# Kernel tuning notes

Measured on AMD Instinct MI355X. Metric: run time of the kernel, lower is better.

The kernel has to match this reference:

```python
import jax, jax.numpy as jnp
import numpy as np

TOPK = 2
NORM_TOPK = True
SCALE = 1.0
EPS = 1e-9


def setup_inputs() -> dict:
    key = jax.random.key(0)
    ks = jax.random.split(key, 9)
    h, i, E = 2048, 1024, 16
    std = 0.02
    return {
        "x": jax.random.normal(ks[0], (1, 2048, h), jnp.float32),
        "Wr": jax.random.normal(ks[1], (E, h), jnp.float32) * std,
        "bias": jnp.zeros((E,), jnp.float32),
        "Wg": jax.random.normal(ks[2], (E, h, i), jnp.float32) * std,
        "Wu": jax.random.normal(ks[3], (E, h, i), jnp.float32) * std,
        "Wd": jax.random.normal(ks[4], (E, i, h), jnp.float32) * std,
        "sWg": jax.random.normal(ks[5], (h, i), jnp.float32) * std,
        "sWu": jax.random.normal(ks[6], (h, i), jnp.float32) * std,
        "sWd": jax.random.normal(ks[7], (i, h), jnp.float32) * std,
    }


def reference(x, Wr, bias, Wg, Wu, Wd, sWg, sWu, sWd):
    b, s, h = x.shape
    E = Wr.shape[0]
    xt = x.reshape(b * s, h)  # [T, h]

    # Router: softmax over expert logits, then top-k
    logits = xt @ Wr.T + bias  # [T, E]
    probs = jax.nn.softmax(logits, axis=-1)
    topk_val, topk_idx = jax.lax.top_k(probs, TOPK)  # [T, K]
    if NORM_TOPK:
        w = topk_val / (jnp.sum(topk_val, axis=-1, keepdims=True) + EPS)
    else:
        w = topk_val
    w = w * SCALE

    # Dense per-expert SwiGLU (mathematically identical to gather/scatter dispatch)
    g = jnp.einsum('th,ehi->tei', xt, Wg)  # [T, E, i]
    u = jnp.einsum('th,ehi->tei', xt, Wu)
    y = jnp.einsum('tei,eih->teh', jax.nn.silu(g) * u, Wd)  # [T, E, h]

    # Combine: out[t] = sum_k w[t,k] * y[t, idx[t,k]]
    oh = jax.nn.one_hot(topk_idx, E, dtype=x.dtype)  # [T, K, E]
    routed = jnp.einsum('tke,tk,teh->th', oh, w, y)

    # Shared expert (SwiGLU)
    shared = (jax.nn.silu(xt @ sWg) * (xt @ sWu)) @ sWd

    return (routed + shared).reshape(b, s, h)
```

## Files before the change

### kernel.cpp

```cpp
#include <hip/hip_runtime.h>
#include <hip/hip_bf16.h>

#define T_TOK 2048
#define HDIM  2048
#define IDIM  1024
#define NE    16
#define NEX   17
#define NASSIGN (T_TOK*3)

#define G1_RT 16
#define G1_NCT 8
#define G2_RT 16
#define G2_NCT 16

typedef __attribute__((ext_vector_type(8))) short bf16x8;
typedef __attribute__((ext_vector_type(4))) float f32x4;

__device__ __forceinline__ unsigned short f2bf(float f) {
    union { float f; unsigned u; } v; v.f = f;
    unsigned r = v.u + 0x7fffu + ((v.u >> 16) & 1u);
    return (unsigned short)(r >> 16);
}
__device__ __forceinline__ unsigned pack2f(float a, float b) {
    __hip_bfloat162 h = __float22bfloat162_rn(float2{a, b});
    unsigned r;
    __builtin_memcpy(&r, &h, 4);
    return r;
}
__device__ __forceinline__ float fidx(const float4& v, int j) {
    return ((const float*)&v)[j];
}
__device__ __forceinline__ int SW(int r) { return (r ^ (r >> 2)) & 7; }
__device__ __forceinline__ int lds_off(int row, int kelem) {
    return (row << 7) + ((((kelem >> 3) ^ SW(row))) << 4) + ((kelem & 7) << 1);
}
__device__ __forceinline__ f32x4 mfma16(bf16x8 a, bf16x8 b, f32x4 c) {
    return __builtin_amdgcn_mfma_f32_16x16x32_bf16(a, b, c, 0, 0, 0);
}
__device__ __forceinline__ void gload_lds16(const void* g, void* lds) {
    __builtin_amdgcn_global_load_lds(
        (const __attribute__((address_space(1))) unsigned*)g,
        (__attribute__((address_space(3))) unsigned*)lds, 16, 0, 0);
}

__global__ __launch_bounds__(256) void k_cvt(const float* __restrict__ x,
                                             unsigned short* __restrict__ xbf) {
    int i = blockIdx.x * 256 + threadIdx.x;
    float4 v = ((const float4*)x)[i];
    uint2 p{pack2f(v.x, v.y), pack2f(v.z, v.w)};
    ((uint2*)xbf)[i] = p;
}

__global__ void k_router(const float* __restrict__ x, const float* __restrict__ Wr,
                         const float* __restrict__ bias, float* __restrict__ wtok,
                         int* __restrict__ idxtok, int* __restrict__ counts) {
    int t = blockIdx.x;
    int lane = threadIdx.x & 63;
    int wave = threadIdx.x >> 6;
    __shared__ float lg[NE];
    const float4* xr = (const float4*)(x + (size_t)t * HDIM);
    for (int e = wave; e < NE; e += 4) {
        const float4* wr = (const float4*)(Wr + (size_t)e * HDIM);
        float s = 0.f;
        for (int j = lane; j < HDIM / 4; j += 64) {
            float4 a = xr[j], b = wr[j];
            s += a.x*b.x + a.y*b.y + a.z*b.z + a.w*b.w;
        }
        #pragma unroll
        for (int d = 32; d; d >>= 1) s += __shfl_xor(s, d);
        if (lane == 0) lg[e] = s + bias[e];
    }
    __syncthreads();
    if (threadIdx.x == 0) {
        float m = lg[0];
        #pragma unroll
        for (int e = 1; e < NE; e++) m = fmaxf(m, lg[e]);
        float p[NE]; float S = 0.f;
        #pragma unroll
        for (int e = 0; e < NE; e++) { p[e] = expf(lg[e] - m); S += p[e]; }
        int i0 = 0;
        #pragma unroll
        for (int e = 1; e < NE; e++) if (p[e] > p[i0]) i0 = e;
        int i1 = (i0 == 0) ? 1 : 0;
        for (int e = 0; e < NE; e++) if (e != i0 && p[e] > p[i1]) i1 = e;
        float v0 = p[i0] / S, v1 = p[i1] / S;
        float wsum = v0 + v1 + 1e-9f;
        wtok[t*2+0] = v0 / wsum;
        wtok[t*2+1] = v1 / wsum;
        idxtok[t*2+0] = i0;
        idxtok[t*2+1] = i1;
        atomicAdd(&counts[i0], 1);
        atomicAdd(&counts[i1], 1);
    }
}

__global__ void k_scan(const int* __restrict__ counts, int* __restrict__ offs,
                       int* __restrict__ cursor) {
    if (threadIdx.x == 0) {
        int acc = 0;
        for (int e = 0; e < NEX; e++) {
            offs[e] = acc; cursor[e] = acc;
            acc += (e < NE) ? counts[e] : T_TOK;
        }
        offs[NEX] = acc;
    }
}

__global__ void k_scatter(const int* __restrict__ idxtok, const float* __restrict__ wtok,
                          int* __restrict__ cursor, const int* __restrict__ offs,
                          int* __restrict__ rows, float* __restrict__ wrow) {
    int t = blockIdx.x * blockDim.x + threadIdx.x;
    if (t >= T_TOK) return;
    #pragma unroll
    for (int k = 0; k < 2; k++) {
        int e = idxtok[t*2+k];
        int pos = atomicAdd(&cursor[e], 1);
        rows[pos] = t;
        wrow[pos] = wtok[t*2+k];
    }
    int p16 = offs[NE] + t;
    rows[p16] = t;
    wrow[p16] = 1.0f;
}

__global__ __launch_bounds__(512) void k_gemm1(
        const unsigned short* __restrict__ xbf,
        const float* __restrict__ Wg, const float* __restrict__ Wu,
        const float* __restrict__ sWg, const float* __restrict__ sWu,
        const int* __restrict__ offs, const int* __restrict__ rows,
        const float* __restrict__ wrow, unsigned short* __restrict__ act) {
    const int nwg = G1_NCT * NEX * G1_RT;
    int bid = blockIdx.x;
    int wg = (bid & 7) * (nwg >> 3) + (bid >> 3);
    int rt = wg & (G1_RT - 1);
    int rest = wg >> 4;
    int e = rest % NEX;
    int ct = rest / NEX;

    int rs = offs[e] + rt * 128;
    int re = offs[e + 1];
    if (rs >= re) return;
    int nrows = min(128, re - rs);
    const float* wgp = (e < NE) ? Wg + (size_t)e * HDIM * IDIM : sWg;
    const float* wup = (e < NE) ? Wu + (size_t)e * HDIM * IDIM : sWu;
    int n0 = ct * 128;

    __shared__ unsigned short As[128 * 64];
    __shared__ unsigned short Bs[128 * 64];
    __shared__ unsigned short Us[128 * 64];
    __shared__ int rloc[128];

    int tid = threadIdx.x;
    if (tid < 128) rloc[tid] = rows[rs + min(tid, nrows - 1)];
    __syncthreads();

    int l = tid & 63, w = tid >> 6;
    int ar0 = w * 8 + (l >> 3);
    int ar1 = 64 + ar0;
    int ac = l & 7;
    const unsigned short* asrc0 = xbf + (size_t)rloc[ar0] * HDIM + ((ac ^ SW(ar0)) << 3);
    const unsigned short* asrc1 = xbf + (size_t)rloc[ar1] * HDIM + ((ac ^ SW(ar1)) << 3);

    int n4 = (tid & 31) << 2;
    int k4 = (tid >> 5) << 2;
    const float* gsrc = wgp + (size_t)k4 * IDIM + n0 + n4;
    const float* usrc = wup + (size_t)k4 * IDIM + n0 + n4;

    int wr = (w >> 2) << 6;
    int wc = (w & 3) << 5;
    int fr = l & 15;
    int fk = (l >> 4) << 3;

    f32x4 accg[4][2] = {}, accu[4][2] = {};

    for (int k0 = 0; k0 < HDIM; k0 += 64) {
        float4 gv[4], uv[4];
        #pragma unroll
        for (int j = 0; j < 4; ++j) gv[j] = *(const float4*)(gsrc + (size_t)(k0 + j) * IDIM);
        #pragma unroll
        for (int j = 0; j < 4; ++j) uv[j] = *(const float4*)(usrc + (size_t)(k0 + j) * IDIM);

        __syncthreads();
        gload_lds16(asrc0 + k0, (char*)As + w * 1024);
        gload_lds16(asrc1 + k0, (char*)As + 8192 + w * 1024);
        #pragma unroll
        for (int i = 0; i < 4; ++i) {
            int n = n4 + i;
            int off = (n << 7) + ((((k4 >> 3) ^ SW(n))) << 4) + ((k4 & 4) << 1);
            uint2 pg{pack2f(fidx(gv[0], i), fidx(gv[1], i)), pack2f(fidx(gv[2], i), fidx(gv[3], i))};
            uint2 pu{pack2f(fidx(uv[0], i), fidx(uv[1], i)), pack2f(fidx(uv[2], i), fidx(uv[3], i))};
            *(uint2*)((char*)Bs + off) = pg;
            *(uint2*)((char*)Us + off) = pu;
        }
        __syncthreads();

        #pragma unroll
        for (int kh = 0; kh < 2; ++kh) {
            int kk = (kh << 5) + fk;
            bf16x8 a[4], bg[2], bu[2];
            #pragma unroll
            for (int m = 0; m < 4; ++m)
                a[m] = *(const bf16x8*)((const char*)As + lds_off(wr + m * 16 + fr, kk));
            #pragma unroll
            for (int n = 0; n < 2; ++n) {
                bg[n] = *(const bf16x8*)((const char*)Bs + lds_off(wc + n * 16 + fr, kk));
                bu[n] = *(const bf16x8*)((const char*)Us + lds_off(wc + n * 16 + fr, kk));
            }
            #pragma unroll
            for (int m = 0; m < 4; ++m) {
                #pragma unroll
                for (int n = 0; n < 2; ++n) {
                    accg[m][n] = mfma16(a[m], bg[n], accg[m][n]);
                    accu[m][n] = mfma16(a[m], bu[n], accu[m][n]);
                }
            }
        }
    }

    int crow = (l >> 4) << 2;
    int ccol = l & 15;
    #pragma unroll
    for (int m = 0; m < 4; ++m) {
        #pragma unroll
        for (int reg = 0; reg < 4; ++reg) {
            int r = wr + m * 16 + crow + reg;
            if (r < nrows) {
                float wv = wrow[rs + r];
                size_t base = (size_t)(rs + r) * IDIM + n0 + wc + ccol;
                #pragma unroll
                for (int n = 0; n < 2; ++n) {
                    float g = accg[m][n][reg], u = accu[m][n][reg];
                    act[base + n * 16] = f2bf(g / (1.f + __expf(-g)) * u * wv);
                }
            }
        }
    }
}

__global__ __launch_bounds__(512) void k_gemm2(
        const unsigned short* __restrict__ act,
        const float* __restrict__ Wd, const float* __restrict__ sWd,
        const int* __restrict__ offs, const int* __restrict__ rows,
        float* __restrict__ out) {
    const int nwg = G2_NCT * NEX * G2_RT;
    int bid = blockIdx.x;
    int wg = (bid & 7) * (nwg >> 3) + (bid >> 3);
    int rt = wg & (G2_RT - 1);
    int rest = wg >> 4;
    int e = rest % NEX;
    int ct = rest / NEX;

    int rs = offs[e] + rt * 128;
    int re = offs[e + 1];
    if (rs >= re) return;
    int nrows = min(128, re - rs);
    const float* wdp = (e < NE) ? Wd + (size_t)e * IDIM * HDIM : sWd;
    int n0 = ct * 128;

    __shared__ unsigned short As[128 * 64];
    __shared__ unsigned short Bs[128 * 64];
    __shared__ int rloc[128];

    int tid = threadIdx.x;
    if (tid < 128) rloc[tid] = rows[rs + min(tid, nrows - 1)];

    int l = tid & 63, w = tid >> 6;
    int ar0 = w * 8 + (l >> 3);
    int ar1 = 64 + ar0;
    int ac = l & 7;
    const unsigned short* asrc0 = act + (size_t)(rs + ar0) * IDIM + ((ac ^ SW(ar0)) << 3);
    const unsigned short* asrc1 = act + (size_t)(rs + ar1) * IDIM + ((ac ^ SW(ar1)) << 3);

    int n4 = (tid & 31) << 2;
    int k4 = (tid >> 5) << 2;
    const float* dsrc = wdp + (size_t)k4 * HDIM + n0 + n4;

    int wr = (w >> 2) << 6;
    int wc = (w & 3) << 5;
    int fr = l & 15;
    int fk = (l >> 4) << 3;

    f32x4 acc[4][2] = {};
    __syncthreads();

    for (int k0 = 0; k0 < IDIM; k0 += 64) {
        float4 dv[4];
        #pragma unroll
        for (int j = 0; j < 4; ++j) dv[j] = *(const float4*)(dsrc + (size_t)(k0 + j) * HDIM);

        __syncthreads();
        gload_lds16(asrc0 + k0, (char*)As + w * 1024);
        gload_lds16(asrc1 + k0, (char*)As + 8192 + w * 1024);
        #pragma unroll
        for (int i = 0; i < 4; ++i) {
            int n = n4 + i;
            int off = (n << 7) + ((((k4 >> 3) ^ SW(n))) << 4) + ((k4 & 4) << 1);
            uint2 pd{pack2f(fidx(dv[0], i), fidx(dv[1], i)), pack2f(fidx(dv[2], i), fidx(dv[3], i))};
            *(uint2*)((char*)Bs + off) = pd;
        }
        __syncthreads();

        #pragma unroll
        for (int kh = 0; kh < 2; ++kh) {
            int kk = (kh << 5) + fk;
            bf16x8 a[4], b[2];
            #pragma unroll
            for (int m = 0; m < 4; ++m)
                a[m] = *(const bf16x8*)((const char*)As + lds_off(wr + m * 16 + fr, kk));
            #pragma unroll
            for (int n = 0; n < 2; ++n)
                b[n] = *(const bf16x8*)((const char*)Bs + lds_off(wc + n * 16 + fr, kk));
            #pragma unroll
            for (int m = 0; m < 4; ++m) {
                #pragma unroll
                for (int n = 0; n < 2; ++n)
                    acc[m][n] = mfma16(a[m], b[n], acc[m][n]);
            }
        }
    }

    int crow = (l >> 4) << 2;
    int ccol = l & 15;
    #pragma unroll
    for (int m = 0; m < 4; ++m) {
        #pragma unroll
        for (int reg = 0; reg < 4; ++reg) {
            int r = wr + m * 16 + crow + reg;
            if (r < nrows) {
                size_t base = (size_t)rloc[r] * HDIM + n0 + wc + ccol;
                atomicAdd(&out[base], acc[m][0][reg]);
                atomicAdd(&out[base + 16], acc[m][1][reg]);
            }
        }
    }
}

extern "C" void kernel_launch(void* const* d_in, const int* in_sizes, int n_in,
                              void* d_out, int out_size, void* d_ws, size_t ws_size,
                              hipStream_t stream) {
    const float* x    = (const float*)d_in[0];
    const float* Wr   = (const float*)d_in[1];
    const float* bias = (const float*)d_in[2];
    const float* Wg   = (const float*)d_in[3];
    const float* Wu   = (const float*)d_in[4];
    const float* Wd   = (const float*)d_in[5];
    const float* sWg  = (const float*)d_in[6];
    const float* sWu  = (const float*)d_in[7];
    const float* sWd  = (const float*)d_in[8];
    float* out = (float*)d_out;

    char* p = (char*)d_ws;
    int*   counts = (int*)p;                 p += 256;
    int*   offs   = (int*)p;                 p += 256;
    int*   cursor = (int*)p;                 p += 256;
    int*   idxtok = (int*)p;                 p += (size_t)T_TOK * 2 * sizeof(int);
    float* wtok   = (float*)p;               p += (size_t)T_TOK * 2 * sizeof(float);
    int*   rows   = (int*)p;                 p += (size_t)NASSIGN * sizeof(int);
    float* wrow   = (float*)p;               p += (size_t)NASSIGN * sizeof(float);
    unsigned short* act = (unsigned short*)p; p += (size_t)NASSIGN * IDIM * sizeof(unsigned short);
    unsigned short* xbf = (unsigned short*)p;

    hipMemsetAsync(counts, 0, 256, stream);
    hipMemsetAsync(d_out, 0, (size_t)out_size * sizeof(float), stream);

    k_cvt<<<dim3(T_TOK * HDIM / 1024), dim3(256), 0, stream>>>(x, xbf);
    k_router<<<dim3(T_TOK), dim3(256), 0, stream>>>(x, Wr, bias, wtok, idxtok, counts);
    k_scan<<<dim3(1), dim3(64), 0, stream>>>(counts, offs, cursor);
    k_scatter<<<dim3((T_TOK + 255) / 256), dim3(256), 0, stream>>>(idxtok, wtok, cursor, offs, rows, wrow);
    k_gemm1<<<dim3(G1_NCT * NEX * G1_RT), dim3(512), 0, stream>>>(xbf, Wg, Wu, sWg, sWu, offs, rows, wrow, act);
    k_gemm2<<<dim3(G2_NCT * NEX * G2_RT), dim3(512), 0, stream>>>(act, Wd, sWd, offs, rows, out);
}
```

Before: 367.8 us.

## Compact tile list, double-buffer LDS, and narrow column tiles in MoE GEMMs

The scan kernel now builds a compact list of 128-row tiles across experts, so GEMM grids launch only real tiles instead of a padded expert-by-row-tile grid full of early-exit blocks. Both GEMMs switch from async global-to-LDS loads to register-staged double buffering: the next K slice is prefetched into registers while MFMAs run on the current LDS buffer. Column tiles shrink from 128 to 64, which doubles the number of workgroups for better CU occupancy. The cost is that each weight tile is reused over fewer columns and the A tile is loaded more often.

```diff
diff --git a/kernel.cpp b/kernel.cpp
--- a/kernel.cpp
+++ b/kernel.cpp
@@ -7,11 +7,12 @@
 #define NE    16
 #define NEX   17
 #define NASSIGN (T_TOK*3)
-
-#define G1_RT 16
-#define G1_NCT 8
-#define G2_RT 16
-#define G2_NCT 16
+#define TM    64
+
+#define G1_NCT 16
+#define G2_NCT 32
+#define G1_NWG (TM*G1_NCT)
+#define G2_NWG (TM*G2_NCT)
 
 typedef __attribute__((ext_vector_type(8))) short bf16x8;
 typedef __attribute__((ext_vector_type(4))) float f32x4;
@@ -36,11 +37,6 @@
 }
 __device__ __forceinline__ f32x4 mfma16(bf16x8 a, bf16x8 b, f32x4 c) {
     return __builtin_amdgcn_mfma_f32_16x16x32_bf16(a, b, c, 0, 0, 0);
-}
-__device__ __forceinline__ void gload_lds16(const void* g, void* lds) {
-    __builtin_amdgcn_global_load_lds(
-        (const __attribute__((address_space(1))) unsigned*)g,
-        (__attribute__((address_space(3))) unsigned*)lds, 16, 0, 0);
 }
 
 __global__ __launch_bounds__(256) void k_cvt(const float* __restrict__ x,
@@ -95,7 +91,7 @@
 }
 
 __global__ void k_scan(const int* __restrict__ counts, int* __restrict__ offs,
-                       int* __restrict__ cursor) {
+                       int* __restrict__ cursor, int4* __restrict__ tiles) {
     if (threadIdx.x == 0) {
         int acc = 0;
         for (int e = 0; e < NEX; e++) {
@@ -103,6 +99,14 @@
             acc += (e < NE) ? counts[e] : T_TOK;
         }
         offs[NEX] = acc;
+        int nt = 0;
+        for (int e = 0; e < NEX; e++) {
+            for (int r = offs[e]; r < offs[e+1]; r += 128) {
+                tiles[nt] = int4{r, min(128, offs[e+1] - r), e, 0};
+                nt++;
+            }
+        }
+        for (; nt < TM; nt++) tiles[nt] = int4{0, 0, 0, 0};
     }
 }
 
@@ -127,93 +131,96 @@
         const unsigned short* __restrict__ xbf,
         const float* __restrict__ Wg, const float* __restrict__ Wu,
         const float* __restrict__ sWg, const float* __restrict__ sWu,
-        const int* __restrict__ offs, const int* __restrict__ rows,
+        const int4* __restrict__ tiles, const int* __restrict__ rows,
         const float* __restrict__ wrow, unsigned short* __restrict__ act) {
-    const int nwg = G1_NCT * NEX * G1_RT;
     int bid = blockIdx.x;
-    int wg = (bid & 7) * (nwg >> 3) + (bid >> 3);
-    int rt = wg & (G1_RT - 1);
-    int rest = wg >> 4;
-    int e = rest % NEX;
-    int ct = rest / NEX;
-
-    int rs = offs[e] + rt * 128;
-    int re = offs[e + 1];
-    if (rs >= re) return;
-    int nrows = min(128, re - rs);
+    int wg = (bid & 7) * (G1_NWG >> 3) + (bid >> 3);
+    int ti = wg & (TM - 1);
+    int ct = wg >> 6;
+
+    int4 tl = tiles[ti];
+    int nrows = tl.y;
+    if (nrows == 0) return;
+    int rs = tl.x, e = tl.z;
     const float* wgp = (e < NE) ? Wg + (size_t)e * HDIM * IDIM : sWg;
     const float* wup = (e < NE) ? Wu + (size_t)e * HDIM * IDIM : sWu;
-    int n0 = ct * 128;
-
-    __shared__ unsigned short As[128 * 64];
-    __shared__ unsigned short Bs[128 * 64];
-    __shared__ unsigned short Us[128 * 64];
+    int n0 = ct * 64;
+
+    __shared__ unsigned short As[2][128 * 64];
+    __shared__ unsigned short Bs[2][64 * 64];
+    __shared__ unsigned short Us[2][64 * 64];
     __shared__ int rloc[128];
 
     int tid = threadIdx.x;
     if (tid < 128) rloc[tid] = rows[rs + min(tid, nrows - 1)];
     __syncthreads();
 
+    int arow = tid >> 2;
+    int akc  = (tid & 3) << 4;
+    const unsigned short* asrc = xbf + (size_t)rloc[arow] * HDIM + akc;
+    int n4 = (tid & 15) << 2;
+    int kb = (tid >> 4) << 1;
+    const float* gsrc = wgp + (size_t)kb * IDIM + n0 + n4;
+    const float* usrc = wup + (size_t)kb * IDIM + n0 + n4;
+
     int l = tid & 63, w = tid >> 6;
-    int ar0 = w * 8 + (l >> 3);
-    int ar1 = 64 + ar0;
-    int ac = l & 7;
-    const unsigned short* asrc0 = xbf + (size_t)rloc[ar0] * HDIM + ((ac ^ SW(ar0)) << 3);
-    const unsigned short* asrc1 = xbf + (size_t)rloc[ar1] * HDIM + ((ac ^ SW(ar1)) << 3);
-
-    int n4 = (tid & 31) << 2;
-    int k4 = (tid >> 5) << 2;
-    const float* gsrc = wgp + (size_t)k4 * IDIM + n0 + n4;
-    const float* usrc = wup + (size_t)k4 * IDIM + n0 + n4;
-
     int wr = (w >> 2) << 6;
-    int wc = (w & 3) << 5;
+    int wc = (w & 3) << 4;
     int fr = l & 15;
     int fk = (l >> 4) << 3;
 
-    f32x4 accg[4][2] = {}, accu[4][2] = {};
-
-    for (int k0 = 0; k0 < HDIM; k0 += 64) {
-        float4 gv[4], uv[4];
-        #pragma unroll
-        for (int j = 0; j < 4; ++j) gv[j] = *(const float4*)(gsrc + (size_t)(k0 + j) * IDIM);
-        #pragma unroll
-        for (int j = 0; j < 4; ++j) uv[j] = *(const float4*)(usrc + (size_t)(k0 + j) * IDIM);
-
-        __syncthreads();
-        gload_lds16(asrc0 + k0, (char*)As + w * 1024);
-        gload_lds16(asrc1 + k0, (char*)As + 8192 + w * 1024);
-        #pragma unroll
-        for (int i = 0; i < 4; ++i) {
-            int n = n4 + i;
-            int off = (n << 7) + ((((k4 >> 3) ^ SW(n))) << 4) + ((k4 & 4) << 1);
-            uint2 pg{pack2f(fidx(gv[0], i), fidx(gv[1], i)), pack2f(fidx(gv[2], i), fidx(gv[3], i))};
-            uint2 pu{pack2f(fidx(uv[0], i), fidx(uv[1], i)), pack2f(fidx(uv[2], i), fidx(uv[3], i))};
-            *(uint2*)((char*)Bs + off) = pg;
-            *(uint2*)((char*)Us + off) = pu;
-        }
-        __syncthreads();
-
+    uint4 aR0, aR1;
+    float4 gR0, gR1, uR0, uR1;
+
+    #define G1_LOAD(K0) do { \
+        aR0 = *(const uint4*)(asrc + (K0)); \
+        aR1 = *(const uint4*)(asrc + (K0) + 8); \
+        gR0 = *(const float4*)(gsrc + (size_t)(K0) * IDIM); \
+        gR1 = *(const float4*)(gsrc + (size_t)(K0) * IDIM + IDIM); \
+        uR0 = *(const float4*)(usrc + (size_t)(K0) * IDIM); \
+        uR1 = *(const float4*)(usrc + (size_t)(K0) * IDIM + IDIM); \
+    } while (0)
+
+    #define G1_WRITE(B) do { \
+        *(uint4*)((char*)As[B] + lds_off(arow, akc))     = aR0; \
+        *(uint4*)((char*)As[B] + lds_off(arow, akc + 8)) = aR1; \
+        _Pragma("unroll") \
+        for (int i = 0; i < 4; ++i) { \
+            int n = n4 + i; \
+            *(unsigned*)((char*)Bs[B] + lds_off(n, kb)) = pack2f(fidx(gR0,i), fidx(gR1,i)); \
+            *(unsigned*)((char*)Us[B] + lds_off(n, kb)) = pack2f(fidx(uR0,i), fidx(uR1,i)); \
+        } \
+    } while (0)
+
+    f32x4 accg[4] = {}, accu[4] = {};
+    const int NK = HDIM / 64;
+
+    G1_LOAD(0);
+    G1_WRITE(0);
+    G1_LOAD(64);
+    __syncthreads();
+
+    for (int k = 0; k < NK; ++k) {
+        int buf = k & 1;
         #pragma unroll
         for (int kh = 0; kh < 2; ++kh) {
             int kk = (kh << 5) + fk;
-            bf16x8 a[4], bg[2], bu[2];
+            bf16x8 a[4], bg, bu;
             #pragma unroll
             for (int m = 0; m < 4; ++m)
-                a[m] = *(const bf16x8*)((const char*)As + lds_off(wr + m * 16 + fr, kk));
-            #pragma unroll
-            for (int n = 0; n < 2; ++n) {
-                bg[n] = *(const bf16x8*)((const char*)Bs + lds_off(wc + n * 16 + fr, kk));
-                bu[n] = *(const bf16x8*)((const char*)Us + lds_off(wc + n * 16 + fr, kk));
-            }
+                a[m] = *(const bf16x8*)((const char*)As[buf] + lds_off(wr + m * 16 + fr, kk));
+            bg = *(const bf16x8*)((const char*)Bs[buf] + lds_off(wc + fr, kk));
+            bu = *(const bf16x8*)((const char*)Us[buf] + lds_off(wc + fr, kk));
             #pragma unroll
             for (int m = 0; m < 4; ++m) {
-                #pragma unroll
-                for (int n = 0; n < 2; ++n) {
-                    accg[m][n] = mfma16(a[m], bg[n], accg[m][n]);
-                    accu[m][n] = mfma16(a[m], bu[n], accu[m][n]);
-                }
+                accg[m] = mfma16(a[m], bg, accg[m]);
+                accu[m] = mfma16(a[m], bu, accu[m]);
             }
+        }
+        if (k + 1 < NK) {
+            G1_WRITE(buf ^ 1);
+            if (k + 2 < NK) G1_LOAD((k + 2) * 64);
+            __syncthreads();
         }
     }
 
@@ -226,12 +233,9 @@
             int r = wr + m * 16 + crow + reg;
             if (r < nrows) {
                 float wv = wrow[rs + r];
-                size_t base = (size_t)(rs + r) * IDIM + n0 + wc + ccol;
-                #pragma unroll
-                for (int n = 0; n < 2; ++n) {
-                    float g = accg[m][n][reg], u = accu[m][n][reg];
-                    act[base + n * 16] = f2bf(g / (1.f + __expf(-g)) * u * wv);
-                }
+                float g = accg[m][reg], u = accu[m][reg];
+                act[(size_t)(rs + r) * IDIM + n0 + wc + ccol] =
+                    f2bf(g / (1.f + __expf(-g)) * u * wv);
             }
         }
     }
@@ -240,82 +244,87 @@
 __global__ __launch_bounds__(512) void k_gemm2(
         const unsigned short* __restrict__ act,
         const float* __restrict__ Wd, const float* __restrict__ sWd,
-        const int* __restrict__ offs, const int* __restrict__ rows,
+        const int4* __restrict__ tiles, const int* __restrict__ rows,
         float* __restrict__ out) {
-    const int nwg = G2_NCT * NEX * G2_RT;
     int bid = blockIdx.x;
-    int wg = (bid & 7) * (nwg >> 3) + (bid >> 3);
-    int rt = wg & (G2_RT - 1);
-    int rest = wg >> 4;
-    int e = rest % NEX;
-    int ct = rest / NEX;
-
-    int rs = offs[e] + rt * 128;
-    int re = offs[e + 1];
-    if (rs >= re) return;
-    int nrows = min(128, re - rs);
+    int wg = (bid & 7) * (G2_NWG >> 3) + (bid >> 3);
+    int ti = wg & (TM - 1);
+    int ct = wg >> 6;
+
+    int4 tl = tiles[ti];
+    int nrows = tl.y;
+    if (nrows == 0) return;
+    int rs = tl.x, e = tl.z;
     const float* wdp = (e < NE) ? Wd + (size_t)e * IDIM * HDIM : sWd;
-    int n0 = ct * 128;
-
-    __shared__ unsigned short As[128 * 64];
-    __shared__ unsigned short Bs[128 * 64];
+    int n0 = ct * 64;
+
+    __shared__ unsigned short As[2][128 * 64];
+    __shared__ unsigned short Bs[2][64 * 64];
     __shared__ int rloc[128];
 
     int tid = threadIdx.x;
     if (tid < 128) rloc[tid] = rows[rs + min(tid, nrows - 1)];
+    __syncthreads();
+
+    int arow = tid >> 2;
+    int akc  = (tid & 3) << 4;
+    const unsigned short* asrc = act + (size_t)(rs + min(arow, nrows - 1)) * IDIM + akc;
+    int n4 = (tid & 15) << 2;
+    int kb = (tid >> 4) << 1;
+    const float* dsrc = wdp + (size_t)kb * HDIM + n0 + n4;
 
     int l = tid & 63, w = tid >> 6;
-    int ar0 = w * 8 + (l >> 3);
-    int ar1 = 64 + ar0;
-    int ac = l & 7;
-    const unsigned short* asrc0 = act + (size_t)(rs + ar0) * IDIM + ((ac ^ SW(ar0)) << 3);
-    const unsigned short* asrc1 = act + (size_t)(rs + ar1) * IDIM + ((ac ^ SW(ar1)) << 3);
-
-    int n4 = (tid & 31) << 2;
-    int k4 = (tid >> 5) << 2;
-    const float* dsrc = wdp + (size_t)k4 * HDIM + n0 + n4;
-
     int wr = (w >> 2) << 6;
-    int wc = (w & 3) << 5;
+    int wc = (w & 3) << 4;
     int fr = l & 15;
     int fk = (l >> 4) << 3;
 
-    f32x4 acc[4][2] = {};
-    __syncthreads();
-
-    for (int k0 = 0; k0 < IDIM; k0 += 64) {
-        float4 dv[4];
-        #pragma unroll
-        for (int j = 0; j < 4; ++j) dv[j] = *(const float4*)(dsrc + (size_t)(k0 + j) * HDIM);
-
-        __syncthreads();
-        gload_lds16(asrc0 + k0, (char*)As + w * 1024);
-        gload_lds16(asrc1 + k0, (char*)As + 8192 + w * 1024);
-        #pragma unroll
-        for (int i = 0; i < 4; ++i) {
-            int n = n4 + i;
-            int off = (n << 7) + ((((k4 >> 3) ^ SW(n))) << 4) + ((k4 & 4) << 1);
-            uint2 pd{pack2f(fidx(dv[0], i), fidx(dv[1], i)), pack2f(fidx(dv[2], i), fidx(dv[3], i))};
-            *(uint2*)((char*)Bs + off) = pd;
-        }
-        __syncthreads();
-
+    uint4 aR0, aR1;
+    float4 dR0, dR1;
+
+    #define G2_LOAD(K0) do { \
+        aR0 = *(const uint4*)(asrc + (K0)); \
+        aR1 = *(const uint4*)(asrc + (K0) + 8); \
+        dR0 = *(const float4*)(dsrc + (size_t)(K0) * HDIM); \
+        dR1 = *(const float4*)(dsrc + (size_t)(K0) * HDIM + HDIM); \
+    } while (0)
+
+    #define G2_WRITE(B) do { \
+        *(uint4*)((char*)As[B] + lds_off(arow, akc))     = aR0; \
+        *(uint4*)((char*)As[B] + lds_off(arow, akc + 8)) = aR1; \
+        _Pragma("unroll") \
+        for (int i = 0; i < 4; ++i) { \
+            int n = n4 + i; \
+            *(unsigned*)((char*)Bs[B] + lds_off(n, kb)) = pack2f(fidx(dR0,i), fidx(dR1,i)); \
+        } \
+    } while (0)
+
+    f32x4 acc[4] = {};
+    const int NK = IDIM / 64;
+
+    G2_LOAD(0);
+    G2_WRITE(0);
+    G2_LOAD(64);
+    __syncthreads();
+
+    for (int k = 0; k < NK; ++k) {
+        int buf = k & 1;
         #pragma unroll
         for (int kh = 0; kh < 2; ++kh) {
             int kk = (kh << 5) + fk;
-            bf16x8 a[4], b[2];
+            bf16x8 a[4], b;
             #pragma unroll
             for (int m = 0; m < 4; ++m)
-                a[m] = *(const bf16x8*)((const char*)As + lds_off(wr + m * 16 + fr, kk));
+                a[m] = *(const bf16x8*)((const char*)As[buf] + lds_off(wr + m * 16 + fr, kk));
+            b = *(const bf16x8*)((const char*)Bs[buf] + lds_off(wc + fr, kk));
             #pragma unroll
-            for (int n = 0; n < 2; ++n)
-                b[n] = *(const bf16x8*)((const char*)Bs + lds_off(wc + n * 16 + fr, kk));
-            #pragma unroll
-            for (int m = 0; m < 4; ++m) {
-                #pragma unroll
-                for (int n = 0; n < 2; ++n)
-                    acc[m][n] = mfma16(a[m], b[n], acc[m][n]);
-            }
+            for (int m = 0; m < 4; ++m)
+                acc[m] = mfma16(a[m], b, acc[m]);
+        }
+        if (k + 1 < NK) {
+            G2_WRITE(buf ^ 1);
+            if (k + 2 < NK) G2_LOAD((k + 2) * 64);
+            __syncthreads();
         }
     }
 
@@ -327,9 +336,7 @@
         for (int reg = 0; reg < 4; ++reg) {
             int r = wr + m * 16 + crow + reg;
             if (r < nrows) {
-                size_t base = (size_t)rloc[r] * HDIM + n0 + wc + ccol;
-                atomicAdd(&out[base], acc[m][0][reg]);
-                atomicAdd(&out[base + 16], acc[m][1][reg]);
+                atomicAdd(&out[(size_t)rloc[r] * HDIM + n0 + wc + ccol], acc[m][reg]);
             }
         }
     }
@@ -353,6 +360,7 @@
     int*   counts = (int*)p;                 p += 256;
     int*   offs   = (int*)p;                 p += 256;
     int*   cursor = (int*)p;                 p += 256;
+    int4*  tiles  = (int4*)p;                p += TM * sizeof(int4);
     int*   idxtok = (int*)p;                 p += (size_t)T_TOK * 2 * sizeof(int);
     float* wtok   = (float*)p;               p += (size_t)T_TOK * 2 * sizeof(float);
     int*   rows   = (int*)p;                 p += (size_t)NASSIGN * sizeof(int);
@@ -365,8 +373,8 @@
 
     k_cvt<<<dim3(T_TOK * HDIM / 1024), dim3(256), 0, stream>>>(x, xbf);
     k_router<<<dim3(T_TOK), dim3(256), 0, stream>>>(x, Wr, bias, wtok, idxtok, counts);
-    k_scan<<<dim3(1), dim3(64), 0, stream>>>(counts, offs, cursor);
+    k_scan<<<dim3(1), dim3(64), 0, stream>>>(counts, offs, cursor, tiles);
     k_scatter<<<dim3((T_TOK + 255) / 256), dim3(256), 0, stream>>>(idxtok, wtok, cursor, offs, rows, wrow);
-    k_gemm1<<<dim3(G1_NCT * NEX * G1_RT), dim3(512), 0, stream>>>(xbf, Wg, Wu, sWg, sWu, offs, rows, wrow, act);
-    k_gemm2<<<dim3(G2_NCT * NEX * G2_RT), dim3(512), 0, stream>>>(act, Wd, sWd, offs, rows, out);
-}
+    k_gemm1<<<dim3(G1_NWG), dim3(512), 0, stream>>>(xbf, Wg, Wu, sWg, sWu, tiles, rows, wrow, act);
+    k_gemm2<<<dim3(G2_NWG), dim3(512), 0, stream>>>(act, Wd, sWd, tiles, rows, out);
+}
```

Result: faster. 318.6 us (-13.4%).
